# Kernel optimization log

Hardware: AMD Instinct MI355X
Metric: run time of the kernel (lower is better)

The kernel has to match this reference:

```python
import jax, jax.numpy as jnp
import numpy as np

N, C, R = 8192, 512, 8
DK = C // R  # 64

def setup_inputs() -> dict:
    key = jax.random.key(0)
    k1, k2, kq, kk, kv = jax.random.split(key, 5)
    s = 0.05
    return {
        "im1": jax.random.normal(k1, (N, C), jnp.float32),
        "im2": jax.random.normal(k2, (N, C), jnp.float32),
        "Wq": jax.random.normal(kq, (C, DK), jnp.float32) * s,
        "Wk": jax.random.normal(kk, (C, DK), jnp.float32) * s,
        "Wv": jax.random.normal(kv, (C, C), jnp.float32) * s,
    }

def reference(im1, im2, Wq, Wk, Wv):
    # shared projections (weights stored as [in, out]; torch Linear is x @ W.T)
    im1_q = im1 @ Wq  # [N, DK]
    im1_k = im1 @ Wk  # [N, DK]
    im1_v = im1 @ Wv  # [N, C]
    im2_q = im2 @ Wq
    im2_k = im2 @ Wk
    im2_v = im2 @ Wv
    # cross attention (no scaling in original)
    im1_attn = jax.nn.softmax(im2_q @ im1_k.T, axis=-1)  # [N, N]
    im2_attn = jax.nn.softmax(im1_q @ im2_k.T, axis=-1)  # [N, N]
    im1_out = im1_attn @ im1_v + im1
    im2_out = im2_attn @ im2_v + im2
    return im1_out, im2_out
```

## Files before the change

kernel.cpp:

```cpp
#include <hip/hip_runtime.h>

#define NN 8192
#define CC 512
#define DKK 64

typedef float f32x4 __attribute__((ext_vector_type(4)));
typedef float f32x16 __attribute__((ext_vector_type(16)));
typedef _Float16 f16x8 __attribute__((ext_vector_type(8)));
typedef _Float16 f16x4 __attribute__((ext_vector_type(4)));

__device__ __forceinline__ f32x4 mfma16(f16x8 a, f16x8 b, f32x4 c) {
    return __builtin_amdgcn_mfma_f32_16x16x32_f16(a, b, c, 0, 0, 0);
}
__device__ __forceinline__ f32x16 mfma32(f16x8 a, f16x8 b, f32x16 c) {
    return __builtin_amdgcn_mfma_f32_32x32x16_f16(a, b, c, 0, 0, 0);
}
__device__ __forceinline__ f16x8 scl8(f16x8 v, float f) {
    _Float16 h = (_Float16)f;
    f16x8 r;
#pragma unroll
    for (int i = 0; i < 8; i++) r[i] = v[i] * h;
    return r;
}

__global__ void wtrans_all_kernel(const float* __restrict__ Wq, const float* __restrict__ Wk,
                                  const float* __restrict__ Wv,
                                  _Float16* __restrict__ Wqt, _Float16* __restrict__ Wkt,
                                  _Float16* __restrict__ Wvf) {
    int idx = blockIdx.x * 256 + threadIdx.x;
    if (idx < 32768) {
        int n = idx >> 9, k = idx & 511;
        Wqt[idx] = (_Float16)Wq[k * 64 + n];
    } else if (idx < 65536) {
        int j = idx - 32768;
        int n = j >> 9, k = j & 511;
        Wkt[j] = (_Float16)Wk[k * 64 + n];
    } else {
        int j = idx - 65536;
        int k16 = j & 15, c = (j >> 4) & 511, ks = j >> 13;
        Wvf[j] = (_Float16)Wv[(size_t)(16 * ks + k16) * 512 + c];
    }
}

__global__ __launch_bounds__(256) void proj_qk2_kernel(
    const float* __restrict__ im1, const float* __restrict__ im2,
    const _Float16* __restrict__ Wqt, const _Float16* __restrict__ Wkt,
    _Float16* __restrict__ Q1, _Float16* __restrict__ Kf1,
    _Float16* __restrict__ Q2, _Float16* __restrict__ Kf2)
{
    const float* X = blockIdx.y ? im2 : im1;
    _Float16* Q = blockIdx.y ? Q2 : Q1;
    _Float16* Kf = blockIdx.y ? Kf2 : Kf1;

    __shared__ __align__(16) _Float16 Wlds[128 * 512];

    const int tid = threadIdx.x;
    const int lane = tid & 63, wave = tid >> 6;
    const int n16 = lane & 15, quad = lane >> 4;

#pragma unroll
    for (int i = 0; i < 32; i++) {
        const int idx = tid + 256 * i;
        const int row = idx >> 6, ch = idx & 63;
        const _Float16* src = (row < 64) ? (Wqt + (size_t)row * 512 + ch * 8)
                                         : (Wkt + (size_t)(row - 64) * 512 + ch * 8);
        *(f16x8*)&Wlds[row * 512 + ((ch ^ (row & 7)) * 8)] = *(const f16x8*)src;
    }
    __syncthreads();

    const int arow = blockIdx.x * 64 + wave * 16 + n16;
    f32x4 acc[8];
#pragma unroll
    for (int i = 0; i < 8; i++) acc[i] = (f32x4){0.f, 0.f, 0.f, 0.f};

    const float* xbase = X + (size_t)arow * 512 + quad * 8;
    for (int kk = 0; kk < 16; kk++) {
        f32x4 xa = *(const f32x4*)(xbase + kk * 32);
        f32x4 xb = *(const f32x4*)(xbase + kk * 32 + 4);
        f16x8 afrag;
#pragma unroll
        for (int j = 0; j < 4; j++) { afrag[j] = (_Float16)xa[j]; afrag[4 + j] = (_Float16)xb[j]; }
#pragma unroll
        for (int t = 0; t < 8; t++) {
            const int row = t * 16 + n16;
            f16x8 bfr = *(const f16x8*)&Wlds[row * 512 + (((4 * kk + quad) ^ (row & 7)) * 8)];
            acc[t] = mfma16(afrag, bfr, acc[t]);
        }
    }
    const int rbase = blockIdx.x * 64 + wave * 16 + quad * 4;
#pragma unroll
    for (int t = 0; t < 4; t++)
#pragma unroll
        for (int r = 0; r < 4; r++) {
            Q[(size_t)(rbase + r) * 64 + t * 16 + n16] = (_Float16)acc[t][r];
            Kf[((size_t)(blockIdx.x * 4 + t) * 64 + (wave * 16 + quad * 4 + r)) * 16 + n16] =
                (_Float16)acc[4 + t][r];
        }
}

__global__ __launch_bounds__(256) void proj_vt_kernel(
    const float* __restrict__ im1, const float* __restrict__ im2,
    const _Float16* __restrict__ Wvf,
    _Float16* __restrict__ Vf1, _Float16* __restrict__ Vf2)
{
    const float* X = blockIdx.y ? im2 : im1;
    _Float16* Vf = blockIdx.y ? Vf2 : Vf1;
    const int n0 = blockIdx.x * 32;
    const int tid = threadIdx.x;
    const int lane = tid & 63, wave = tid >> 6;
    const int l31 = lane & 31, lhi = lane >> 5;

    __shared__ __align__(16) _Float16 Xlds[32 * 512];

#pragma unroll
    for (int i = 0; i < 8; i++) {
        const int n = tid >> 3;
        const int chunk = (tid & 7) + 8 * i;
        const float* xp = X + (size_t)(n0 + n) * CC + chunk * 8;
        f32x4 x0 = *(const f32x4*)xp;
        f32x4 x1 = *(const f32x4*)(xp + 4);
        f16x8 d;
#pragma unroll
        for (int j = 0; j < 4; j++) { d[j] = (_Float16)x0[j]; d[4 + j] = (_Float16)x1[j]; }
        *(f16x8*)&Xlds[n * 512 + ((chunk ^ (n & 7)) * 8)] = d;
    }
    __syncthreads();

    f32x16 acc[4];
#pragma unroll
    for (int t = 0; t < 4; t++)
#pragma unroll
        for (int r = 0; r < 16; r++) acc[t][r] = 0.f;

    for (int ks = 0; ks < 32; ks++) {
        f16x8 xb = *(const f16x8*)&Xlds[l31 * 512 + (((2 * ks + lhi) ^ (l31 & 7)) * 8)];
#pragma unroll
        for (int ct = 0; ct < 4; ct++) {
            const _Float16* wp = Wvf + ((size_t)ks * 512 + 128 * wave + 32 * ct + l31) * 16 + 8 * lhi;
            acc[ct] = mfma32(*(const f16x8*)wp, xb, acc[ct]);
        }
    }
    const int tile = n0 >> 6;
    const int ksbase = (n0 & 32) >> 4;
#pragma unroll
    for (int ct = 0; ct < 4; ct++)
#pragma unroll
        for (int r = 0; r < 16; r++) {
            const int c = 128 * wave + 32 * ct + (r & 3) + 8 * (r >> 2) + 4 * lhi;
            const int ks = ksbase + (l31 >> 4);
            Vf[((size_t)(tile * 4 + ks) * 512 + c) * 16 + (l31 & 15)] = (_Float16)acc[ct][r];
        }
}

__global__ __launch_bounds__(512, 2) void flash5_kernel(
    const _Float16* __restrict__ Q1, const _Float16* __restrict__ Kf1,
    const _Float16* __restrict__ Q2, const _Float16* __restrict__ Kf2,
    const _Float16* __restrict__ Vf1, const _Float16* __restrict__ Vf2,
    const float* __restrict__ im1, const float* __restrict__ im2,
    float* __restrict__ out)
{
    const int img = blockIdx.y;
    const _Float16* Q = img ? Q1 : Q2;
    const _Float16* Kf = img ? Kf2 : Kf1;
    const _Float16* Vf = img ? Vf2 : Vf1;
    const float* res = img ? im2 : im1;
    float* o = out + (size_t)img * NN * CC;

    __shared__ __align__(16) char smem[64 * 516 * 4];
    __shared__ float mPart[2][2][2][64];
    __shared__ float mF[2][2][64], lF[2][2][64];

    const int tid = threadIdx.x;
    const int lane = tid & 63, wave = tid >> 6;
    const int l31 = lane & 31, lhi = lane >> 5;
    const int g = wave >> 2, wg = wave & 3;
    const int b = wg & 1, a = wg >> 1;
    const int qbase = blockIdx.x * 64;

    _Float16* Pbase = (_Float16*)smem;

    f16x8 qf[4];
    {
        const _Float16* qp = Q + (size_t)(qbase + 32 * b + l31) * DKK + 8 * lhi;
#pragma unroll
        for (int k = 0; k < 4; k++) qf[k] = *(const f16x8*)(qp + 16 * k);
    }

    f32x16 acc[8];
#pragma unroll
    for (int t = 0; t < 8; t++)
#pragma unroll
        for (int r = 0; r < 16; r++) acc[t][r] = 0.f;
    float ma_run = -3e38f, l_run = 0.f;
    float mg_run[2] = {-3e38f, -3e38f};

    auto do_qk = [&](int s) {
        const int t = 2 * s + g;
        const int pbuf = s & 1;
        _Float16* Pg = Pbase + (pbuf * 2 + g) * 4096;
        f32x16 sA;
#pragma unroll
        for (int r = 0; r < 16; r++) sA[r] = 0.f;
#pragma unroll
        for (int k = 0; k < 4; k++) {
            f16x8 kf = *(const f16x8*)(Kf + ((size_t)(t * 4 + k) * 64 + 32 * a + l31) * 16 + 8 * lhi);
            sA = mfma32(kf, qf[k], sA);
        }
        float mx = -3e38f;
#pragma unroll
        for (int r = 0; r < 16; r++) mx = fmaxf(mx, sA[r]);
        mx = fmaxf(mx, __shfl_xor(mx, 32));
        const float manew = fmaxf(ma_run, mx);
        if (lane < 32) mPart[pbuf][g][a][32 * b + lane] = manew;
        float ls = 0.f;
#pragma unroll
        for (int r = 0; r < 16; r++) {
            float p = __expf(sA[r] - manew);
            ls += p;
            sA[r] = p;
        }
        ls += __shfl_xor(ls, 32);
        l_run = l_run * __expf(ma_run - manew) + ls;
        ma_run = manew;
        const int q = 32 * b + l31;
#pragma unroll
        for (int gg = 0; gg < 4; gg++) {
            f16x4 p4;
#pragma unroll
            for (int u = 0; u < 4; u++) p4[u] = (_Float16)sA[gg * 4 + u];
            *(f16x4*)&Pg[((4 * a + gg) * 64 + q) * 8 + 4 * lhi] = p4;
        }
    };

    do_qk(0);
    __syncthreads();

    for (int s = 0; s < 64; s++) {
        const int t = 2 * s + g;
        const int pbuf = s & 1;
        _Float16* Pg = Pbase + (pbuf * 2 + g) * 4096;

        f16x8 va01[8];
#pragma unroll
        for (int k = 0; k < 2; k++)
#pragma unroll
            for (int ct = 0; ct < 4; ct++)
                va01[k * 4 + ct] = *(const f16x8*)(Vf +
                    ((size_t)(t * 4 + k) * 512 + 128 * wg + 32 * ct + l31) * 16 + 8 * lhi);

        if (s < 63) do_qk(s + 1);

        float al[2], f0[2], f1[2];
#pragma unroll
        for (int qt = 0; qt < 2; qt++) {
            const int q = 32 * qt + l31;
            const float m0 = mPart[pbuf][g][0][q];
            const float m1 = mPart[pbuf][g][1][q];
            const float mgn = fmaxf(mg_run[qt], fmaxf(m0, m1));
            al[qt] = __expf(mg_run[qt] - mgn);
            f0[qt] = __expf(m0 - mgn);
            f1[qt] = __expf(m1 - mgn);
            mg_run[qt] = mgn;
        }
        if (!__all((al[0] == 1.f) & (al[1] == 1.f))) {
#pragma unroll
            for (int ct = 0; ct < 4; ct++)
#pragma unroll
                for (int r = 0; r < 16; r++) {
                    acc[ct * 2 + 0][r] *= al[0];
                    acc[ct * 2 + 1][r] *= al[1];
                }
        }
        const bool noscale =
            __all((f0[0] == 1.f) & (f1[0] == 1.f) & (f0[1] == 1.f) & (f1[1] == 1.f));
#pragma unroll
        for (int k = 0; k < 4; k++) {
            f16x8 pb0 = *(const f16x8*)&Pg[((2 * k + lhi) * 64 + l31) * 8];
            f16x8 pb1 = *(const f16x8*)&Pg[((2 * k + lhi) * 64 + 32 + l31) * 8];
            if (!noscale) {
                pb0 = scl8(pb0, k < 2 ? f0[0] : f1[0]);
                pb1 = scl8(pb1, k < 2 ? f0[1] : f1[1]);
            }
#pragma unroll
            for (int ct = 0; ct < 4; ct++) {
                f16x8 va;
                if (k < 2) va = va01[k * 4 + ct];
                else va = *(const f16x8*)(Vf +
                    ((size_t)(t * 4 + k) * 512 + 128 * wg + 32 * ct + l31) * 16 + 8 * lhi);
                acc[ct * 2 + 0] = mfma32(va, pb0, acc[ct * 2 + 0]);
                acc[ct * 2 + 1] = mfma32(va, pb1, acc[ct * 2 + 1]);
            }
        }
        __syncthreads();
    }

    if (lane < 32) {
        mF[g][a][32 * b + lane] = ma_run;
        lF[g][a][32 * b + lane] = l_run;
    }
    __syncthreads();

    float fac[2];
#pragma unroll
    for (int qt = 0; qt < 2; qt++) {
        const int q = 32 * qt + l31;
        const float m00 = mF[0][0][q], m01 = mF[0][1][q];
        const float m10 = mF[1][0][q], m11 = mF[1][1][q];
        const float M = fmaxf(fmaxf(m00, m01), fmaxf(m10, m11));
        const float den = lF[0][0][q] * __expf(m00 - M) + lF[0][1][q] * __expf(m01 - M) +
                          lF[1][0][q] * __expf(m10 - M) + lF[1][1][q] * __expf(m11 - M);
        fac[qt] = __expf(mg_run[qt] - M) / den;
    }

    float* Olds = (float*)smem;
    if (g == 0) {
#pragma unroll
        for (int ct = 0; ct < 4; ct++)
#pragma unroll
            for (int qt = 0; qt < 2; qt++)
#pragma unroll
                for (int r = 0; r < 16; r++) {
                    const int c = 128 * wg + 32 * ct + (r & 3) + 8 * (r >> 2) + 4 * lhi;
                    Olds[(32 * qt + l31) * 516 + c] = acc[ct * 2 + qt][r] * fac[qt];
                }
    }
    __syncthreads();
    if (g == 1) {
#pragma unroll
        for (int ct = 0; ct < 4; ct++)
#pragma unroll
            for (int qt = 0; qt < 2; qt++)
#pragma unroll
                for (int r = 0; r < 16; r++) {
                    const int c = 128 * wg + 32 * ct + (r & 3) + 8 * (r >> 2) + 4 * lhi;
                    Olds[(32 * qt + l31) * 516 + c] += acc[ct * 2 + qt][r] * fac[qt];
                }
    }
    __syncthreads();

    {
        const int q = tid >> 3;
        const size_t grow = (size_t)(qbase + q);
#pragma unroll
        for (int i = 0; i < 16; i++) {
            const int cw = ((tid & 7) + 8 * i) * 4;
            f32x4 v = *(const f32x4*)&Olds[q * 516 + cw];
            f32x4 rr = *(const f32x4*)(res + grow * CC + cw);
            v += rr;
            *(f32x4*)(o + grow * CC + cw) = v;
        }
    }
}

extern "C" void kernel_launch(void* const* d_in, const int* in_sizes, int n_in,
                              void* d_out, int out_size, void* d_ws, size_t ws_size,
                              hipStream_t stream) {
    const float* im1 = (const float*)d_in[0];
    const float* im2 = (const float*)d_in[1];
    const float* Wq  = (const float*)d_in[2];
    const float* Wk  = (const float*)d_in[3];
    const float* Wv  = (const float*)d_in[4];
    float* out = (float*)d_out;

    _Float16* w = (_Float16*)d_ws;
    _Float16* Wqt = w;
    _Float16* Wkt = Wqt + 64 * 512;
    _Float16* Wvf = Wkt + 64 * 512;
    _Float16* Q1  = Wvf + 512 * 512;
    _Float16* Kf1 = Q1 + NN * DKK;
    _Float16* Q2  = Kf1 + NN * DKK;
    _Float16* Kf2 = Q2 + NN * DKK;
    _Float16* Vf1 = Kf2 + NN * DKK;
    _Float16* Vf2 = Vf1 + (size_t)CC * NN;

    wtrans_all_kernel<<<1280, 256, 0, stream>>>(Wq, Wk, Wv, Wqt, Wkt, Wvf);
    proj_qk2_kernel<<<dim3(128, 2), 256, 0, stream>>>(im1, im2, Wqt, Wkt, Q1, Kf1, Q2, Kf2);
    proj_vt_kernel<<<dim3(256, 2), 256, 0, stream>>>(im1, im2, Wvf, Vf1, Vf2);
    flash5_kernel<<<dim3(128, 2), 512, 0, stream>>>(Q1, Kf1, Q2, Kf2, Vf1, Vf2, im1, im2, out);
}
```

Measured before the change: 423.2 us.

## Shrink flash tile to 32 queries with four-way key split per block

The attention kernel now handles 32 queries per block instead of 64, launching twice as many blocks (512). The key range is split four ways across wave groups instead of two, and each wave owns a 64-column slice of the output. Accumulator registers drop from 8 to 2 tiles, the LDS output-staging reduction is removed, and results are written straight from registers with the residual added. Launch bounds are raised to allow 4 blocks per CU. In exchange, each V fragment is reused across fewer queries, so global/L2 traffic for V roughly doubles, and per-step max merging reads 8 partial maxima.

```diff
diff --git a/kernel.cpp b/kernel.cpp
--- a/kernel.cpp
+++ b/kernel.cpp
@@ -152,7 +152,7 @@
         }
 }
 
-__global__ __launch_bounds__(512, 2) void flash5_kernel(
+__global__ __launch_bounds__(512, 4) void flash6_kernel(
     const _Float16* __restrict__ Q1, const _Float16* __restrict__ Kf1,
     const _Float16* __restrict__ Q2, const _Float16* __restrict__ Kf2,
     const _Float16* __restrict__ Vf1, const _Float16* __restrict__ Vf2,
@@ -166,52 +166,55 @@
     const float* res = img ? im2 : im1;
     float* o = out + (size_t)img * NN * CC;
 
-    __shared__ __align__(16) char smem[64 * 516 * 4];
-    __shared__ float mPart[2][2][2][64];
-    __shared__ float mF[2][2][64], lF[2][2][64];
+    __shared__ __align__(16) _Float16 P[2][4][8][32][8];
+    __shared__ float mPart[2][4][2][32];
+    __shared__ float mF[4][2][32], lF[4][2][32];
 
     const int tid = threadIdx.x;
-    const int lane = tid & 63, wave = tid >> 6;
+    const int lane = tid & 63, w = tid >> 6;
     const int l31 = lane & 31, lhi = lane >> 5;
-    const int g = wave >> 2, wg = wave & 3;
-    const int b = wg & 1, a = wg >> 1;
-    const int qbase = blockIdx.x * 64;
-
-    _Float16* Pbase = (_Float16*)smem;
+    const int g = w >> 1, a = w & 1;
+    const int qbase = blockIdx.x * 32;
 
     f16x8 qf[4];
     {
-        const _Float16* qp = Q + (size_t)(qbase + 32 * b + l31) * DKK + 8 * lhi;
+        const _Float16* qp = Q + (size_t)(qbase + l31) * DKK + 8 * lhi;
 #pragma unroll
         for (int k = 0; k < 4; k++) qf[k] = *(const f16x8*)(qp + 16 * k);
     }
 
-    f32x16 acc[8];
-#pragma unroll
-    for (int t = 0; t < 8; t++)
+    f32x16 acc[2];
+#pragma unroll
+    for (int t = 0; t < 2; t++)
 #pragma unroll
         for (int r = 0; r < 16; r++) acc[t][r] = 0.f;
+
     float ma_run = -3e38f, l_run = 0.f;
-    float mg_run[2] = {-3e38f, -3e38f};
+    float mg_run = -3e38f;
+
+    const _Float16* kb = Kf + ((size_t)(32 * a + l31)) * 16 + 8 * lhi;
+    const _Float16* vb = Vf + ((size_t)(64 * w + l31)) * 16 + 8 * lhi;
 
     auto do_qk = [&](int s) {
-        const int t = 2 * s + g;
+        const int t = 4 * s + g;
         const int pbuf = s & 1;
-        _Float16* Pg = Pbase + (pbuf * 2 + g) * 4096;
         f32x16 sA;
 #pragma unroll
         for (int r = 0; r < 16; r++) sA[r] = 0.f;
 #pragma unroll
         for (int k = 0; k < 4; k++) {
-            f16x8 kf = *(const f16x8*)(Kf + ((size_t)(t * 4 + k) * 64 + 32 * a + l31) * 16 + 8 * lhi);
+            f16x8 kf = *(const f16x8*)(kb + (size_t)(t * 4 + k) * (64 * 16));
             sA = mfma32(kf, qf[k], sA);
         }
-        float mx = -3e38f;
-#pragma unroll
-        for (int r = 0; r < 16; r++) mx = fmaxf(mx, sA[r]);
+        float mr[8];
+#pragma unroll
+        for (int i = 0; i < 8; i++) mr[i] = fmaxf(sA[i], sA[i + 8]);
+#pragma unroll
+        for (int i = 0; i < 4; i++) mr[i] = fmaxf(mr[i], mr[i + 4]);
+        float mx = fmaxf(fmaxf(mr[0], mr[1]), fmaxf(mr[2], mr[3]));
         mx = fmaxf(mx, __shfl_xor(mx, 32));
         const float manew = fmaxf(ma_run, mx);
-        if (lane < 32) mPart[pbuf][g][a][32 * b + lane] = manew;
+        if (lane < 32) mPart[pbuf][g][a][lane] = manew;
         float ls = 0.f;
 #pragma unroll
         for (int r = 0; r < 16; r++) {
@@ -222,134 +225,102 @@
         ls += __shfl_xor(ls, 32);
         l_run = l_run * __expf(ma_run - manew) + ls;
         ma_run = manew;
-        const int q = 32 * b + l31;
 #pragma unroll
         for (int gg = 0; gg < 4; gg++) {
             f16x4 p4;
 #pragma unroll
             for (int u = 0; u < 4; u++) p4[u] = (_Float16)sA[gg * 4 + u];
-            *(f16x4*)&Pg[((4 * a + gg) * 64 + q) * 8 + 4 * lhi] = p4;
+            *(f16x4*)&P[pbuf][g][4 * a + gg][l31][4 * lhi] = p4;
         }
     };
 
     do_qk(0);
     __syncthreads();
 
-    for (int s = 0; s < 64; s++) {
-        const int t = 2 * s + g;
+    for (int s = 0; s < 32; s++) {
         const int pbuf = s & 1;
-        _Float16* Pg = Pbase + (pbuf * 2 + g) * 4096;
-
-        f16x8 va01[8];
-#pragma unroll
-        for (int k = 0; k < 2; k++)
-#pragma unroll
-            for (int ct = 0; ct < 4; ct++)
-                va01[k * 4 + ct] = *(const f16x8*)(Vf +
-                    ((size_t)(t * 4 + k) * 512 + 128 * wg + 32 * ct + l31) * 16 + 8 * lhi);
-
-        if (s < 63) do_qk(s + 1);
-
-        float al[2], f0[2], f1[2];
-#pragma unroll
-        for (int qt = 0; qt < 2; qt++) {
-            const int q = 32 * qt + l31;
-            const float m0 = mPart[pbuf][g][0][q];
-            const float m1 = mPart[pbuf][g][1][q];
-            const float mgn = fmaxf(mg_run[qt], fmaxf(m0, m1));
-            al[qt] = __expf(mg_run[qt] - mgn);
-            f0[qt] = __expf(m0 - mgn);
-            f1[qt] = __expf(m1 - mgn);
-            mg_run[qt] = mgn;
-        }
-        if (!__all((al[0] == 1.f) & (al[1] == 1.f))) {
-#pragma unroll
-            for (int ct = 0; ct < 4; ct++)
-#pragma unroll
-                for (int r = 0; r < 16; r++) {
-                    acc[ct * 2 + 0][r] *= al[0];
-                    acc[ct * 2 + 1][r] *= al[1];
+
+        f16x8 va0[8];
+#pragma unroll
+        for (int tt = 0; tt < 4; tt++)
+#pragma unroll
+            for (int ct = 0; ct < 2; ct++)
+                va0[tt * 2 + ct] = *(const f16x8*)(vb +
+                    ((size_t)((4 * s + tt) * 4) * 512 + 32 * ct) * 16);
+
+        if (s < 31) do_qk(s + 1);
+
+        float f[4][2];
+        float mgn = mg_run;
+#pragma unroll
+        for (int g2 = 0; g2 < 4; g2++)
+#pragma unroll
+            for (int a2 = 0; a2 < 2; a2++) {
+                f[g2][a2] = mPart[pbuf][g2][a2][l31];
+                mgn = fmaxf(mgn, f[g2][a2]);
+            }
+        const float al = __expf(mg_run - mgn);
+        mg_run = mgn;
+        if (!__all(al == 1.f)) {
+#pragma unroll
+            for (int t = 0; t < 2; t++)
+#pragma unroll
+                for (int r = 0; r < 16; r++) acc[t][r] *= al;
+        }
+        bool nos1 = true;
+#pragma unroll
+        for (int g2 = 0; g2 < 4; g2++)
+#pragma unroll
+            for (int a2 = 0; a2 < 2; a2++) {
+                f[g2][a2] = __expf(f[g2][a2] - mgn);
+                nos1 &= (f[g2][a2] == 1.f);
+            }
+        const bool nos = __all(nos1);
+
+#pragma unroll
+        for (int tt = 0; tt < 4; tt++)
+#pragma unroll
+            for (int k = 0; k < 4; k++) {
+                f16x8 pb = *(const f16x8*)&P[pbuf][tt][2 * k + lhi][l31][0];
+                if (!nos) pb = scl8(pb, f[tt][k >> 1]);
+#pragma unroll
+                for (int ct = 0; ct < 2; ct++) {
+                    f16x8 va = (k == 0) ? va0[tt * 2 + ct]
+                        : *(const f16x8*)(vb +
+                            ((size_t)((4 * s + tt) * 4 + k) * 512 + 32 * ct) * 16);
+                    acc[ct] = mfma32(va, pb, acc[ct]);
                 }
-        }
-        const bool noscale =
-            __all((f0[0] == 1.f) & (f1[0] == 1.f) & (f0[1] == 1.f) & (f1[1] == 1.f));
-#pragma unroll
-        for (int k = 0; k < 4; k++) {
-            f16x8 pb0 = *(const f16x8*)&Pg[((2 * k + lhi) * 64 + l31) * 8];
-            f16x8 pb1 = *(const f16x8*)&Pg[((2 * k + lhi) * 64 + 32 + l31) * 8];
-            if (!noscale) {
-                pb0 = scl8(pb0, k < 2 ? f0[0] : f1[0]);
-                pb1 = scl8(pb1, k < 2 ? f0[1] : f1[1]);
             }
-#pragma unroll
-            for (int ct = 0; ct < 4; ct++) {
-                f16x8 va;
-                if (k < 2) va = va01[k * 4 + ct];
-                else va = *(const f16x8*)(Vf +
-                    ((size_t)(t * 4 + k) * 512 + 128 * wg + 32 * ct + l31) * 16 + 8 * lhi);
-                acc[ct * 2 + 0] = mfma32(va, pb0, acc[ct * 2 + 0]);
-                acc[ct * 2 + 1] = mfma32(va, pb1, acc[ct * 2 + 1]);
-            }
-        }
         __syncthreads();
     }
 
     if (lane < 32) {
-        mF[g][a][32 * b + lane] = ma_run;
-        lF[g][a][32 * b + lane] = l_run;
+        mF[g][a][lane] = ma_run;
+        lF[g][a][lane] = l_run;
     }
     __syncthreads();
 
-    float fac[2];
-#pragma unroll
-    for (int qt = 0; qt < 2; qt++) {
-        const int q = 32 * qt + l31;
-        const float m00 = mF[0][0][q], m01 = mF[0][1][q];
-        const float m10 = mF[1][0][q], m11 = mF[1][1][q];
-        const float M = fmaxf(fmaxf(m00, m01), fmaxf(m10, m11));
-        const float den = lF[0][0][q] * __expf(m00 - M) + lF[0][1][q] * __expf(m01 - M) +
-                          lF[1][0][q] * __expf(m10 - M) + lF[1][1][q] * __expf(m11 - M);
-        fac[qt] = __expf(mg_run[qt] - M) / den;
-    }
-
-    float* Olds = (float*)smem;
-    if (g == 0) {
-#pragma unroll
-        for (int ct = 0; ct < 4; ct++)
-#pragma unroll
-            for (int qt = 0; qt < 2; qt++)
-#pragma unroll
-                for (int r = 0; r < 16; r++) {
-                    const int c = 128 * wg + 32 * ct + (r & 3) + 8 * (r >> 2) + 4 * lhi;
-                    Olds[(32 * qt + l31) * 516 + c] = acc[ct * 2 + qt][r] * fac[qt];
-                }
-    }
-    __syncthreads();
-    if (g == 1) {
-#pragma unroll
-        for (int ct = 0; ct < 4; ct++)
-#pragma unroll
-            for (int qt = 0; qt < 2; qt++)
-#pragma unroll
-                for (int r = 0; r < 16; r++) {
-                    const int c = 128 * wg + 32 * ct + (r & 3) + 8 * (r >> 2) + 4 * lhi;
-                    Olds[(32 * qt + l31) * 516 + c] += acc[ct * 2 + qt][r] * fac[qt];
-                }
-    }
-    __syncthreads();
-
-    {
-        const int q = tid >> 3;
-        const size_t grow = (size_t)(qbase + q);
-#pragma unroll
-        for (int i = 0; i < 16; i++) {
-            const int cw = ((tid & 7) + 8 * i) * 4;
-            f32x4 v = *(const f32x4*)&Olds[q * 516 + cw];
-            f32x4 rr = *(const f32x4*)(res + grow * CC + cw);
-            v += rr;
-            *(f32x4*)(o + grow * CC + cw) = v;
-        }
-    }
+    const float M = mg_run;
+    float den = 0.f;
+#pragma unroll
+    for (int g2 = 0; g2 < 4; g2++)
+#pragma unroll
+        for (int a2 = 0; a2 < 2; a2++)
+            den += lF[g2][a2][l31] * __expf(mF[g2][a2][l31] - M);
+    const float fac = 1.f / den;
+
+#pragma unroll
+    for (int ct = 0; ct < 2; ct++)
+#pragma unroll
+        for (int rg = 0; rg < 4; rg++) {
+            const int c = 64 * w + 32 * ct + 8 * rg + 4 * lhi;
+            const size_t off = (size_t)(qbase + l31) * CC + c;
+            f32x4 v;
+#pragma unroll
+            for (int u = 0; u < 4; u++) v[u] = acc[ct][4 * rg + u] * fac;
+            f32x4 r4 = *(const f32x4*)(res + off);
+            *(f32x4*)(o + off) = v + r4;
+        }
 }
 
 extern "C" void kernel_launch(void* const* d_in, const int* in_sizes, int n_in,
@@ -376,5 +347,5 @@
     wtrans_all_kernel<<<1280, 256, 0, stream>>>(Wq, Wk, Wv, Wqt, Wkt, Wvf);
     proj_qk2_kernel<<<dim3(128, 2), 256, 0, stream>>>(im1, im2, Wqt, Wkt, Q1, Kf1, Q2, Kf2);
     proj_vt_kernel<<<dim3(256, 2), 256, 0, stream>>>(im1, im2, Wvf, Vf1, Vf2);
-    flash5_kernel<<<dim3(128, 2), 512, 0, stream>>>(Q1, Kf1, Q2, Kf2, Vf1, Vf2, im1, im2, out);
-}
+    flash6_kernel<<<dim3(256, 2), 512, 0, stream>>>(Q1, Kf1, Q2, Kf2, Vf1, Vf2, im1, im2, out);
+}
```

Measured after the change: 356.5 us. 15.8% less time.
